# Kernel optimization log

Measured on AMD Instinct MI355X. Metric: run time of the kernel, lower is better.

The kernel has to match this reference:

```python
import jax, jax.numpy as jnp
import numpy as np

DIM = 384; H = 64; W = 64; WS = 4; NH = 6; SHIFT = 2
L = WS * WS          # 16 tokens per window
DH = DIM // NH       # 64
SCALE = DH ** -0.5
MLP_H = int(DIM * 4.0)
NW = (H // WS) * (W // WS)


def _ln(x, g, b):
    m = x.mean(-1, keepdims=True)
    v = ((x - m) ** 2).mean(-1, keepdims=True)
    return (x - m) / jnp.sqrt(v + 1e-5) * g + b


def _win(x, B):
    # (B, N, C) -> (B*nW, L, C)
    x = x.reshape(B, H // WS, WS, W // WS, WS, DIM)
    x = x.transpose(0, 1, 3, 2, 4, 5)
    return x.reshape(B * NW, L, DIM)


def _unwin(xw, B):
    # (B*nW, L, C) -> (B, N, C)
    x = xw.reshape(B, H // WS, W // WS, WS, WS, DIM)
    x = x.transpose(0, 1, 3, 2, 4, 5)
    return x.reshape(B, H * W, DIM)


def _build_mask():
    img = np.zeros((H, W))
    slices = [slice(0, -WS), slice(-WS, -SHIFT), slice(-SHIFT, None)]
    cnt = 0
    for hs in slices:
        for ws_ in slices:
            img[hs, ws_] = cnt
            cnt += 1
    mw = img.reshape(H // WS, WS, W // WS, WS).transpose(0, 2, 1, 3).reshape(-1, L)
    am = mw[:, None, :] - mw[:, :, None]          # (nW, L, L)
    am = np.where(am != 0, -100.0, 0.0).astype(np.float32)
    return jnp.asarray(am)

ATTN_MASK = _build_mask()  # (nW, L, L)


def setup_inputs() -> dict:
    key = jax.random.key(0)
    ks = jax.random.split(key, 16)
    n = lambda k, s: jax.random.normal(k, s, jnp.float32) * 0.02
    inp = {
        'x_main': jax.random.normal(ks[0], (16, H * W, DIM), jnp.float32),
        'x_mpmt': jax.random.normal(ks[1], (16, H * W, DIM), jnp.float32),
        'g_q': jnp.ones((DIM,)), 'b_q': jnp.zeros((DIM,)),
        'g_km': jnp.ones((DIM,)), 'b_km': jnp.zeros((DIM,)),
        'g_kp': jnp.ones((DIM,)), 'b_kp': jnp.zeros((DIM,)),
        'Wq': n(ks[2], (DIM, DIM)), 'bq': jnp.zeros((DIM,)),
        'Wk': n(ks[3], (DIM, DIM)), 'bk': jnp.zeros((DIM,)),
        'Wv': n(ks[4], (DIM, DIM)), 'bv': jnp.zeros((DIM,)),
        'Wo': n(ks[5], (DIM, DIM)), 'bo': jnp.zeros((DIM,)),
        'g_mlp': jnp.ones((DIM,)), 'b_mlp': jnp.zeros((DIM,)),
        'W1': n(ks[6], (DIM, MLP_H)), 'b1': jnp.zeros((MLP_H,)),
        'W2': n(ks[7], (MLP_H, DIM)), 'b2': jnp.zeros((DIM,)),
    }
    return inp


def reference(x_main, x_mpmt, g_q, b_q, g_km, b_km, g_kp, b_kp,
              Wq, bq, Wk, bk, Wv, bv, Wo, bo, g_mlp, b_mlp, W1, b1, W2, b2):
    B, N, C = x_main.shape
    q = _ln(x_main, g_q, b_q)
    km = _ln(x_main, g_km, b_km)
    kp = _ln(x_mpmt, g_kp, b_kp)

    roll = lambda t: jnp.roll(t.reshape(B, H, W, C), (-SHIFT, -SHIFT), axis=(1, 2)).reshape(B, N, C)
    q, km, kp = roll(q), roll(km), roll(kp)

    q_w = _win(q, B)                                  # (B*nW, L, C)
    kv_w = jnp.concatenate([_win(km, B), _win(kp, B)], axis=1)  # (B*nW, 2L, C)

    def heads(x, Wm, bm):
        y = x @ Wm + bm
        return y.reshape(y.shape[0], y.shape[1], NH, DH).transpose(0, 2, 1, 3)

    Q = heads(q_w, Wq, bq)    # (B*nW, h, L, dh)
    K = heads(kv_w, Wk, bk)   # (B*nW, h, 2L, dh)
    V = heads(kv_w, Wv, bv)

    scores = jnp.einsum('whqd,whkd->whqk', Q, K) * SCALE   # (B*nW, h, L, 2L)
    mask2 = jnp.concatenate([ATTN_MASK, ATTN_MASK], axis=-1)  # (nW, L, 2L)
    scores = scores.reshape(B, NW, NH, L, 2 * L) + mask2[None, :, None]
    attn = jax.nn.softmax(scores.reshape(B * NW, NH, L, 2 * L), axis=-1)

    out = jnp.einsum('whqk,whkd->whqd', attn, V)           # (B*nW, h, L, dh)
    out = out.transpose(0, 2, 1, 3).reshape(B * NW, L, C)
    y = _unwin(out, B)
    y = jnp.roll(y.reshape(B, H, W, C), (SHIFT, SHIFT), axis=(1, 2)).reshape(B, N, C)

    x = x_main + (y @ Wo + bo)
    xm = _ln(x, g_mlp, b_mlp)
    x = x + (jax.nn.gelu(xm @ W1 + b1, approximate=False) @ W2 + b2)
    return x
```

## Files before the change

### kernel.cpp

```cpp
#include <hip/hip_runtime.h>
#include <cstdint>
#include <cstddef>

#define DEVI __device__ __forceinline__

typedef __attribute__((ext_vector_type(8))) short bf16x8;
typedef __attribute__((ext_vector_type(4))) float f32x4;

DEVI unsigned short f2bf(float f) {
  unsigned u = __builtin_bit_cast(unsigned, f);
  u += 0x7fffu + ((u >> 16) & 1u);
  return (unsigned short)(u >> 16);
}

DEVI f32x4 mfma16(bf16x8 a, bf16x8 b, f32x4 c) {
  return __builtin_amdgcn_mfma_f32_16x16x32_bf16(a, b, c, 0, 0, 0);
}

#define GLD16(g, l) __builtin_amdgcn_global_load_lds( \
    (const __attribute__((address_space(1))) unsigned int*)(g), \
    (__attribute__((address_space(3))) unsigned int*)(l), 16, 0, 0)

__global__ __launch_bounds__(256)
void wtrans_all(const float* __restrict__ Wq, const float* __restrict__ Wk,
                const float* __restrict__ Wv, const float* __restrict__ Wo,
                const float* __restrict__ W1, const float* __restrict__ W2,
                unsigned short* __restrict__ out) {
  __shared__ float tl[32][33];
  int tu = blockIdx.x;
  const float* W;
  int K, N, obase;
  if (tu < 576) {
    int m = tu / 144;
    W = (m == 0) ? Wq : (m == 1) ? Wk : (m == 2) ? Wv : Wo;
    K = 384; N = 384; obase = m * 147456; tu -= m * 144;
  } else if (tu < 1152) {
    W = W1; K = 384; N = 1536; obase = 589824; tu -= 576;
  } else {
    W = W2; K = 1536; N = 384; obase = 1179648; tu -= 1152;
  }
  const int ktiles = K >> 5;
  const int tn = tu / ktiles, tk = tu - tn * ktiles;
  const int c = threadIdx.x & 31, rq = threadIdx.x >> 5;
#pragma unroll
  for (int ph = 0; ph < 4; ++ph) {
    int kk = tk * 32 + ph * 8 + rq;
    tl[ph * 8 + rq][c] = W[(size_t)kk * N + tn * 32 + c];
  }
  __syncthreads();
#pragma unroll
  for (int ph = 0; ph < 4; ++ph) {
    int nn = tn * 32 + ph * 8 + rq;
    out[obase + (size_t)nn * K + tk * 32 + c] = f2bf(tl[c][ph * 8 + rq]);
  }
}

__global__ __launch_bounds__(256)
void ln_win_k(const float* __restrict__ xm, const float* __restrict__ xp,
              const float* __restrict__ gq, const float* __restrict__ bq,
              const float* __restrict__ gkm, const float* __restrict__ bkm,
              const float* __restrict__ gkp, const float* __restrict__ bkp,
              unsigned short* __restrict__ q_ln,
              unsigned short* __restrict__ kv_ln, int wbase) {
  const int dl = blockIdx.x * 4 + (threadIdx.x >> 6);
  const int l = threadIdx.x & 63;
  const int wl = dl >> 4, t = dl & 15;
  const int w = wbase + wl;
  const int b = w >> 8, wi = w & 255;
  const int hs = (((wi >> 4) << 2) + (t >> 2) + 2) & 63;
  const int ws2 = (((wi & 15) << 2) + (t & 3) + 2) & 63;
  const size_t src = ((size_t)b * 4096 + hs * 64 + ws2) * 384;
  float am[6], ap[6];
  float s1 = 0, s2 = 0, s3 = 0, s4 = 0;
#pragma unroll
  for (int j = 0; j < 6; ++j) {
    am[j] = xm[src + l + j * 64];
    ap[j] = xp[src + l + j * 64];
    s1 += am[j]; s2 += am[j] * am[j];
    s3 += ap[j]; s4 += ap[j] * ap[j];
  }
#pragma unroll
  for (int o = 1; o < 64; o <<= 1) {
    s1 += __shfl_xor(s1, o); s2 += __shfl_xor(s2, o);
    s3 += __shfl_xor(s3, o); s4 += __shfl_xor(s4, o);
  }
  const float mm = s1 * (1.f / 384.f);
  const float vm = s2 * (1.f / 384.f) - mm * mm;
  const float rm = rsqrtf(vm + 1e-5f);
  const float mp = s3 * (1.f / 384.f);
  const float vp = s4 * (1.f / 384.f) - mp * mp;
  const float rp = rsqrtf(vp + 1e-5f);
  unsigned short* qrow = q_ln + (size_t)dl * 384;
  unsigned short* kmrow = kv_ln + ((size_t)wl * 32 + t) * 384;
  unsigned short* kprow = kmrow + 16 * 384;
#pragma unroll
  for (int j = 0; j < 6; ++j) {
    int c = l + j * 64;
    float nm = (am[j] - mm) * rm;
    float np = (ap[j] - mp) * rp;
    qrow[c] = f2bf(nm * gq[c] + bq[c]);
    kmrow[c] = f2bf(nm * gkm[c] + bkm[c]);
    kprow[c] = f2bf(np * gkp[c] + bkp[c]);
  }
}

__global__ __launch_bounds__(256)
void ln_k(const float* __restrict__ x, const float* __restrict__ g,
          const float* __restrict__ b, unsigned short* __restrict__ o) {
  const int row = blockIdx.x * 4 + (threadIdx.x >> 6);
  const int l = threadIdx.x & 63;
  const float* xr = x + (size_t)row * 384;
  float a[6];
  float s1 = 0, s2 = 0;
#pragma unroll
  for (int j = 0; j < 6; ++j) {
    a[j] = xr[l + j * 64];
    s1 += a[j]; s2 += a[j] * a[j];
  }
#pragma unroll
  for (int of = 1; of < 64; of <<= 1) {
    s1 += __shfl_xor(s1, of); s2 += __shfl_xor(s2, of);
  }
  const float m = s1 * (1.f / 384.f);
  const float v = s2 * (1.f / 384.f) - m * m;
  const float r = rsqrtf(v + 1e-5f);
  unsigned short* orow = o + (size_t)row * 384;
#pragma unroll
  for (int j = 0; j < 6; ++j) {
    int c = l + j * 64;
    orow[c] = f2bf((a[j] - m) * r * g[c] + b[c]);
  }
}

enum { EPI_BF16 = 0, EPI_KV = 1, EPI_WO = 2, EPI_GELU = 3, EPI_W2 = 4 };

template <int EPI>
__global__ __launch_bounds__(256, 2)
void gemm_k(const unsigned short* __restrict__ A,
            const unsigned short* __restrict__ Bt,
            const float* __restrict__ bias, const float* __restrict__ bias2,
            void* __restrict__ Cv, void* __restrict__ Cv2,
            const float* __restrict__ extra, int wbase, int M, int N, int K) {
  __shared__ unsigned short As[2][128 * 32];
  __shared__ unsigned short Bs[2][128 * 32];
  const int tid = threadIdx.x;
  const int l = tid & 63, wv = tid >> 6;
  const int lr = l & 15, og = l >> 4;

  const unsigned gx = gridDim.x;
  const unsigned nwg = gx * gridDim.y;
  unsigned idx = blockIdx.y * gx + blockIdx.x;
  idx = (idx & 7u) * (nwg >> 3) + (idx >> 3);
  const int m0 = (int)(idx / gx) * 128, n0 = (int)(idx % gx) * 128;

  const int wm = (wv >> 1) * 64, wn = (wv & 1) * 64;

  f32x4 acc[4][4];
#pragma unroll
  for (int i = 0; i < 4; ++i)
#pragma unroll
    for (int j = 0; j < 4; ++j) acc[i][j] = (f32x4){0.f, 0.f, 0.f, 0.f};

  const int r0 = tid >> 2, o0 = (tid & 3) * 8;
  const unsigned short* a0 = A + (size_t)(m0 + r0) * K + o0;
  const unsigned short* a1 = a0 + (size_t)64 * K;
  const unsigned short* b0 = Bt + (size_t)(n0 + r0) * K + o0;
  const unsigned short* b1 = b0 + (size_t)64 * K;
  const int lo = wv * 512;

  const int nk = K >> 5;
  GLD16(a0, &As[0][lo]);
  GLD16(a1, &As[0][2048 + lo]);
  GLD16(b0, &Bs[0][lo]);
  GLD16(b1, &Bs[0][2048 + lo]);
  __syncthreads();

  for (int t = 0; t < nk; ++t) {
    const int cur = t & 1;
    if (t + 1 < nk) {
      const int k0 = (t + 1) << 5;
      GLD16(a0 + k0, &As[cur ^ 1][lo]);
      GLD16(a1 + k0, &As[cur ^ 1][2048 + lo]);
      GLD16(b0 + k0, &Bs[cur ^ 1][lo]);
      GLD16(b1 + k0, &Bs[cur ^ 1][2048 + lo]);
    }
    bf16x8 af[4], bfr[4];
#pragma unroll
    for (int i = 0; i < 4; ++i)
      af[i] = *(const bf16x8*)&As[cur][(wm + i * 16 + lr) * 32 + og * 8];
#pragma unroll
    for (int j = 0; j < 4; ++j)
      bfr[j] = *(const bf16x8*)&Bs[cur][(wn + j * 16 + lr) * 32 + og * 8];
#pragma unroll
    for (int i = 0; i < 4; ++i)
#pragma unroll
      for (int j = 0; j < 4; ++j)
        acc[i][j] = mfma16(af[i], bfr[j], acc[i][j]);
    __syncthreads();
  }

  float bvj[4];
#pragma unroll
  for (int j = 0; j < 4; ++j) {
    int c = n0 + wn + j * 16 + lr;
    bvj[j] = (EPI == EPI_KV) ? (c < 384 ? bias[c] : bias2[c - 384]) : bias[c];
  }
  const int cb = n0 + wn + lr;

  if constexpr (EPI == EPI_BF16) {
    unsigned short* C = (unsigned short*)Cv;
#pragma unroll
    for (int i = 0; i < 4; ++i) {
      const int rb = m0 + wm + i * 16 + og * 4;
#pragma unroll
      for (int r = 0; r < 4; ++r) {
        unsigned short* row = C + (size_t)(rb + r) * N + cb;
#pragma unroll
        for (int j = 0; j < 4; ++j) row[j * 16] = f2bf(acc[i][j][r] + bvj[j]);
      }
    }
  } else if constexpr (EPI == EPI_GELU) {
    unsigned short* C = (unsigned short*)Cv;
#pragma unroll
    for (int i = 0; i < 4; ++i) {
      const int rb = m0 + wm + i * 16 + og * 4;
#pragma unroll
      for (int r = 0; r < 4; ++r) {
        unsigned short* row = C + (size_t)(rb + r) * N + cb;
#pragma unroll
        for (int j = 0; j < 4; ++j) {
          float v = acc[i][j][r] + bvj[j];
          v = 0.5f * v * (1.f + erff(v * 0.70710678118654752f));
          row[j * 16] = f2bf(v);
        }
      }
    }
  } else if constexpr (EPI == EPI_WO) {
    float* C = (float*)Cv;
#pragma unroll
    for (int i = 0; i < 4; ++i) {
      const int rb = m0 + wm + i * 16 + og * 4;
#pragma unroll
      for (int r = 0; r < 4; ++r) {
        int rr = rb + r;
        int wdx = (rr >> 4) + wbase, t = rr & 15;
        int b = wdx >> 8, wi = wdx & 255;
        int hd = (((wi >> 4) << 2) + (t >> 2) + 2) & 63;
        int wd = (((wi & 15) << 2) + (t & 3) + 2) & 63;
        size_t dst = ((size_t)b * 4096 + hd * 64 + wd) * 384 + cb;
#pragma unroll
        for (int j = 0; j < 4; ++j)
          C[dst + j * 16] = extra[dst + j * 16] + acc[i][j][r] + bvj[j];
      }
    }
  } else if constexpr (EPI == EPI_W2) {
    float* C = (float*)Cv;
#pragma unroll
    for (int i = 0; i < 4; ++i) {
      const int rb = m0 + wm + i * 16 + og * 4;
#pragma unroll
      for (int r = 0; r < 4; ++r) {
        size_t ix = (size_t)(rb + r) * N + cb;
#pragma unroll
        for (int j = 0; j < 4; ++j)
          C[ix + j * 16] = extra[ix + j * 16] + acc[i][j][r] + bvj[j];
      }
    }
  } else {
    if (n0 + wn < 384) {
      unsigned short* C = (unsigned short*)Cv;
#pragma unroll
      for (int i = 0; i < 4; ++i) {
        const int rb = m0 + wm + i * 16 + og * 4;
#pragma unroll
        for (int r = 0; r < 4; ++r) {
          unsigned short* row = C + (size_t)(rb + r) * 384 + cb;
#pragma unroll
          for (int j = 0; j < 4; ++j)
            row[j * 16] = f2bf(acc[i][j][r] + bvj[j]);
        }
      }
    } else {
      unsigned short* C = (unsigned short*)Cv2;
#pragma unroll
      for (int j = 0; j < 4; ++j) {
        const int cc = n0 + wn + j * 16 + lr - 384;
#pragma unroll
        for (int i = 0; i < 4; ++i) {
          const int rb = m0 + wm + i * 16 + og * 4;
          int wdx = rb >> 5, u = rb & 31;
          size_t ix = (((size_t)wdx * 6 + (cc >> 6)) * 64 + (cc & 63)) * 32 + u;
          ushort4 v4;
          v4.x = f2bf(acc[i][j][0] + bvj[j]);
          v4.y = f2bf(acc[i][j][1] + bvj[j]);
          v4.z = f2bf(acc[i][j][2] + bvj[j]);
          v4.w = f2bf(acc[i][j][3] + bvj[j]);
          *(ushort4*)&C[ix] = v4;
        }
      }
    }
  }
}

__global__ __launch_bounds__(384)
void attn_k(const unsigned short* __restrict__ Q,
            const unsigned short* __restrict__ K,
            const unsigned short* __restrict__ Vt,
            unsigned short* __restrict__ O, int wbase) {
  __shared__ unsigned short P_lds[6][16][32];
  const int wl = blockIdx.x;
  const int h = threadIdx.x >> 6, l = threadIdx.x & 63;
  const int lr = l & 15, og = l >> 4;
  const int wi = (wbase + wl) & 255;
  const int wh4 = (wi >> 4) << 2, ww4 = (wi & 15) << 2;

  auto rid = [&](int t) -> int {
    int hp = wh4 + (t >> 2), wp = ww4 + (t & 3);
    int rh = hp < 60 ? 0 : (hp < 62 ? 1 : 2);
    int rw = wp < 60 ? 0 : (wp < 62 ? 1 : 2);
    return rh * 3 + rw;
  };
  const int ridq = rid(lr);

  const size_t qbase = ((size_t)wl * 16 + lr) * 384 + h * 64 + og * 8;
  bf16x8 qf0 = *(const bf16x8*)&Q[qbase];
  bf16x8 qf1 = *(const bf16x8*)&Q[qbase + 32];
  const size_t kbase = ((size_t)wl * 32 + lr) * 384 + h * 64 + og * 8;
  bf16x8 kf00 = *(const bf16x8*)&K[kbase];
  bf16x8 kf01 = *(const bf16x8*)&K[kbase + 32];
  bf16x8 kf10 = *(const bf16x8*)&K[kbase + 16 * 384];
  bf16x8 kf11 = *(const bf16x8*)&K[kbase + 16 * 384 + 32];

  f32x4 s0 = (f32x4){0.f, 0.f, 0.f, 0.f}, s1 = (f32x4){0.f, 0.f, 0.f, 0.f};
  s0 = mfma16(kf00, qf0, s0);
  s0 = mfma16(kf01, qf1, s0);
  s1 = mfma16(kf10, qf0, s1);
  s1 = mfma16(kf11, qf1, s1);

  float p[8];
  float mx = -1e30f;
#pragma unroll
  for (int r = 0; r < 4; ++r) {
    float msk = (rid(og * 4 + r) == ridq) ? 0.f : -100.f;
    p[r] = s0[r] * 0.125f + msk;
    p[r + 4] = s1[r] * 0.125f + msk;
    mx = fmaxf(mx, fmaxf(p[r], p[r + 4]));
  }
  mx = fmaxf(mx, __shfl_xor(mx, 16));
  mx = fmaxf(mx, __shfl_xor(mx, 32));
  float sum = 0.f;
#pragma unroll
  for (int r = 0; r < 8; ++r) {
    p[r] = __expf(p[r] - mx);
    sum += p[r];
  }
  sum += __shfl_xor(sum, 16);
  sum += __shfl_xor(sum, 32);
  const float inv = 1.f / sum;

  uint2 pk;
  pk.x = (unsigned)f2bf(p[0] * inv) | ((unsigned)f2bf(p[1] * inv) << 16);
  pk.y = (unsigned)f2bf(p[2] * inv) | ((unsigned)f2bf(p[3] * inv) << 16);
  *(uint2*)&P_lds[h][lr][og * 4] = pk;
  pk.x = (unsigned)f2bf(p[4] * inv) | ((unsigned)f2bf(p[5] * inv) << 16);
  pk.y = (unsigned)f2bf(p[6] * inv) | ((unsigned)f2bf(p[7] * inv) << 16);
  *(uint2*)&P_lds[h][lr][16 + og * 4] = pk;

  bf16x8 pf = *(const bf16x8*)&P_lds[h][lr][og * 8];

  const size_t vbase = (((size_t)wl * 6 + h) * 64 + lr) * 32 + og * 8;
  f32x4 o4[4];
#pragma unroll
  for (int f = 0; f < 4; ++f) {
    bf16x8 vf = *(const bf16x8*)&Vt[vbase + (size_t)f * 16 * 32];
    o4[f] = mfma16(pf, vf, (f32x4){0.f, 0.f, 0.f, 0.f});
  }
#pragma unroll
  for (int f = 0; f < 4; ++f)
#pragma unroll
    for (int r = 0; r < 4; ++r)
      O[((size_t)wl * 16 + og * 4 + r) * 384 + h * 64 + f * 16 + lr] =
          f2bf(o4[f][r]);
}

extern "C" void kernel_launch(void* const* d_in, const int* in_sizes, int n_in,
                              void* d_out, int out_size, void* d_ws,
                              size_t ws_size, hipStream_t stream) {
  const float* x_main = (const float*)d_in[0];
  const float* x_mpmt = (const float*)d_in[1];
  const float* g_q = (const float*)d_in[2];
  const float* b_q = (const float*)d_in[3];
  const float* g_km = (const float*)d_in[4];
  const float* b_km = (const float*)d_in[5];
  const float* g_kp = (const float*)d_in[6];
  const float* b_kp = (const float*)d_in[7];
  const float* Wq = (const float*)d_in[8];
  const float* bq = (const float*)d_in[9];
  const float* Wk = (const float*)d_in[10];
  const float* bk = (const float*)d_in[11];
  const float* Wv = (const float*)d_in[12];
  const float* bv = (const float*)d_in[13];
  const float* Wo = (const float*)d_in[14];
  const float* bo = (const float*)d_in[15];
  const float* g_mlp = (const float*)d_in[16];
  const float* b_mlp = (const float*)d_in[17];
  const float* W1 = (const float*)d_in[18];
  const float* b1 = (const float*)d_in[19];
  const float* W2 = (const float*)d_in[20];
  const float* b2 = (const float*)d_in[21];

  char* ws = (char*)d_ws;
  unsigned short* q_ln = (unsigned short*)(ws + 0);
  unsigned short* Qb = (unsigned short*)(ws + 25165824ull);
  unsigned short* Kb = (unsigned short*)(ws + 50331648ull);
  unsigned short* Vtb = (unsigned short*)(ws + 100663296ull);
  unsigned short* attn_out = q_ln;
  unsigned short* xm = (unsigned short*)(ws + 0);
  unsigned short* Hb = (unsigned short*)(ws + 50331648ull);
  unsigned short* wt = (unsigned short*)(ws + 150994944ull);
  unsigned short* Wqt = wt + 0;
  unsigned short* Wkvt = wt + 147456;
  unsigned short* Wot = wt + 442368;
  unsigned short* W1t = wt + 589824;
  unsigned short* W2t = wt + 1179648;
  float* xout = (float*)d_out;

  wtrans_all<<<1728, 256, 0, stream>>>(Wq, Wk, Wv, Wo, W1, W2, wt);

  for (int c = 0; c < 2; ++c) {
    const int wbase = c * 2048;
    unsigned short* kvl =
        (unsigned short*)((char*)d_out + (size_t)c * 50331648ull);

    ln_win_k<<<8192, 256, 0, stream>>>(x_main, x_mpmt, g_q, b_q, g_km, b_km,
                                       g_kp, b_kp, q_ln, kvl, wbase);

    gemm_k<EPI_BF16><<<dim3(3, 256), 256, 0, stream>>>(
        q_ln, Wqt, bq, nullptr, Qb, nullptr, nullptr, 0, 32768, 384, 384);

    gemm_k<EPI_KV><<<dim3(6, 512), 256, 0, stream>>>(
        kvl, Wkvt, bk, bv, Kb, Vtb, nullptr, 0, 65536, 768, 384);

    attn_k<<<2048, 384, 0, stream>>>(Qb, Kb, Vtb, attn_out, wbase);

    gemm_k<EPI_WO><<<dim3(3, 256), 256, 0, stream>>>(
        attn_out, Wot, bo, nullptr, xout, nullptr, x_main, wbase, 32768, 384,
        384);
  }

  ln_k<<<16384, 256, 0, stream>>>(xout, g_mlp, b_mlp, xm);

  for (int hhalf = 0; hhalf < 2; ++hhalf) {
    const size_t ro = (size_t)hhalf * 32768;
    gemm_k<EPI_GELU><<<dim3(12, 256), 256, 0, stream>>>(
        xm + ro * 384, W1t, b1, nullptr, Hb, nullptr, nullptr, 0, 32768, 1536,
        384);
    gemm_k<EPI_W2><<<dim3(3, 256), 256, 0, stream>>>(
        Hb, W2t, b2, nullptr, xout + ro * 384, nullptr, xout + ro * 384, 0,
        32768, 384, 1536);
  }
}
```

Baseline: 823.4 us.

## Triple-buffer GEMM LDS with swizzled layout and use polynomial erf for GELU

The GEMM mainloop goes from double to triple buffering. Explicit vmcnt waits and barriers keep two tiles in flight while one is computed. LDS column chunks are XOR-swizzled to reduce bank conflicts on the MFMA fragment reads. The GELU epilogue swaps erff for an Abramowitz-Stegun polynomial with a fast reciprocal and exp, which is cheaper but approximate to about 1e-7 absolute error. More LDS per block (48KB) may reduce occupancy.

Result: no change. 830.8 us (+0.9%).

```diff
diff --git a/kernel.cpp b/kernel.cpp
--- a/kernel.cpp
+++ b/kernel.cpp
@@ -15,6 +15,17 @@
 
 DEVI f32x4 mfma16(bf16x8 a, bf16x8 b, f32x4 c) {
   return __builtin_amdgcn_mfma_f32_16x16x32_bf16(a, b, c, 0, 0, 0);
+}
+
+DEVI float gelu_f(float x) {
+  float z = __builtin_fabsf(x) * 0.70710678118654752f;
+  float t = __builtin_amdgcn_rcpf(1.f + 0.3275911f * z);
+  float p = t * (0.254829592f +
+            t * (-0.284496736f +
+            t * (1.421413741f + t * (-1.453152027f + t * 1.061405429f))));
+  float er = 1.f - p * __expf(-z * z);
+  er = __builtin_copysignf(er, x);
+  return 0.5f * x * (1.f + er);
 }
 
 #define GLD16(g, l) __builtin_amdgcn_global_load_lds( \
@@ -141,8 +152,8 @@
             const float* __restrict__ bias, const float* __restrict__ bias2,
             void* __restrict__ Cv, void* __restrict__ Cv2,
             const float* __restrict__ extra, int wbase, int M, int N, int K) {
-  __shared__ unsigned short As[2][128 * 32];
-  __shared__ unsigned short Bs[2][128 * 32];
+  __shared__ unsigned short As[3][128 * 32];
+  __shared__ unsigned short Bs[3][128 * 32];
   const int tid = threadIdx.x;
   const int l = tid & 63, wv = tid >> 6;
   const int lr = l & 15, og = l >> 4;
@@ -161,43 +172,57 @@
 #pragma unroll
     for (int j = 0; j < 4; ++j) acc[i][j] = (f32x4){0.f, 0.f, 0.f, 0.f};
 
-  const int r0 = tid >> 2, o0 = (tid & 3) * 8;
-  const unsigned short* a0 = A + (size_t)(m0 + r0) * K + o0;
+  const int r0 = tid >> 2;
+  const int o0s = (((tid & 3) ^ ((tid >> 3) & 3)) * 8);
+  const unsigned short* a0 = A + (size_t)(m0 + r0) * K + o0s;
   const unsigned short* a1 = a0 + (size_t)64 * K;
-  const unsigned short* b0 = Bt + (size_t)(n0 + r0) * K + o0;
+  const unsigned short* b0 = Bt + (size_t)(n0 + r0) * K + o0s;
   const unsigned short* b1 = b0 + (size_t)64 * K;
   const int lo = wv * 512;
-
-  const int nk = K >> 5;
-  GLD16(a0, &As[0][lo]);
-  GLD16(a1, &As[0][2048 + lo]);
-  GLD16(b0, &Bs[0][lo]);
-  GLD16(b1, &Bs[0][2048 + lo]);
-  __syncthreads();
-
-  for (int t = 0; t < nk; ++t) {
-    const int cur = t & 1;
-    if (t + 1 < nk) {
-      const int k0 = (t + 1) << 5;
-      GLD16(a0 + k0, &As[cur ^ 1][lo]);
-      GLD16(a1 + k0, &As[cur ^ 1][2048 + lo]);
-      GLD16(b0 + k0, &Bs[cur ^ 1][lo]);
-      GLD16(b1 + k0, &Bs[cur ^ 1][2048 + lo]);
-    }
+  const int ogs = (og ^ ((lr >> 1) & 3)) * 8;
+
+  auto stage = [&](int kt, int buf) {
+    const int k0 = kt << 5;
+    GLD16(a0 + k0, &As[buf][lo]);
+    GLD16(a1 + k0, &As[buf][2048 + lo]);
+    GLD16(b0 + k0, &Bs[buf][lo]);
+    GLD16(b1 + k0, &Bs[buf][2048 + lo]);
+  };
+  auto compute = [&](int buf) {
     bf16x8 af[4], bfr[4];
 #pragma unroll
     for (int i = 0; i < 4; ++i)
-      af[i] = *(const bf16x8*)&As[cur][(wm + i * 16 + lr) * 32 + og * 8];
+      af[i] = *(const bf16x8*)&As[buf][(wm + i * 16 + lr) * 32 + ogs];
 #pragma unroll
     for (int j = 0; j < 4; ++j)
-      bfr[j] = *(const bf16x8*)&Bs[cur][(wn + j * 16 + lr) * 32 + og * 8];
+      bfr[j] = *(const bf16x8*)&Bs[buf][(wn + j * 16 + lr) * 32 + ogs];
 #pragma unroll
     for (int i = 0; i < 4; ++i)
 #pragma unroll
       for (int j = 0; j < 4; ++j)
         acc[i][j] = mfma16(af[i], bfr[j], acc[i][j]);
-    __syncthreads();
-  }
+  };
+
+  const int nk = K >> 5;
+  stage(0, 0);
+  stage(1, 1);
+  for (int t = 0; t < nk - 2; ++t) {
+    stage(t + 2, (t + 2) % 3);
+    asm volatile("s_waitcnt vmcnt(8)" ::: "memory");
+    __builtin_amdgcn_s_barrier();
+    compute(t % 3);
+    asm volatile("" ::: "memory");
+    __builtin_amdgcn_s_barrier();
+    asm volatile("" ::: "memory");
+  }
+  asm volatile("s_waitcnt vmcnt(4)" ::: "memory");
+  __builtin_amdgcn_s_barrier();
+  compute((nk - 2) % 3);
+  asm volatile("" ::: "memory");
+  __builtin_amdgcn_s_barrier();
+  asm volatile("s_waitcnt vmcnt(0)" ::: "memory");
+  __builtin_amdgcn_s_barrier();
+  compute((nk - 1) % 3);
 
   float bvj[4];
 #pragma unroll
@@ -228,11 +253,8 @@
       for (int r = 0; r < 4; ++r) {
         unsigned short* row = C + (size_t)(rb + r) * N + cb;
 #pragma unroll
-        for (int j = 0; j < 4; ++j) {
-          float v = acc[i][j][r] + bvj[j];
-          v = 0.5f * v * (1.f + erff(v * 0.70710678118654752f));
-          row[j * 16] = f2bf(v);
-        }
+        for (int j = 0; j < 4; ++j)
+          row[j * 16] = f2bf(gelu_f(acc[i][j][r] + bvj[j]));
       }
     }
   } else if constexpr (EPI == EPI_WO) {
```
